# Kernel tuning notes

Hardware: AMD Instinct MI355X
Metric: run time of the kernel (lower is better)

Reference implementation:

```python
import jax, jax.numpy as jnp
import numpy as np


def setup_inputs() -> dict:
    key = jax.random.key(0)
    k1, k2, k3 = jax.random.split(key, 3)
    bs, chart_len, H = 256, 1024, 256
    num_steps, start_index = 512, 512
    chart = jax.random.normal(k1, (bs, chart_len, 2 * H), dtype=jnp.float32)
    operations = jax.random.randint(k2, (num_steps, bs, 2), 0, start_index, dtype=jnp.int64)
    U = jax.random.normal(k3, (5 * H, 2 * H), dtype=jnp.float32) * 0.05
    b = jnp.zeros((5 * H,), dtype=jnp.float32)
    return {"chart": chart, "operations": operations, "start_index": start_index, "U": U, "b": b}


def reference(chart, operations, start_index, U, b):
    H = U.shape[0] // 5
    bs = chart.shape[0]
    batch_idx = jnp.arange(bs)
    num_steps = operations.shape[0]

    def step_fn(ch, xs):
        step, ops = xs
        left = ch[batch_idx, ops[:, 0]]   # [bs, 2H]
        right = ch[batch_idx, ops[:, 1]]  # [bs, 2H]
        ccL, ccR = left[:, :H], right[:, :H]
        hh = jnp.concatenate([left[:, H:], right[:, H:]], axis=-1)  # [bs, 2H]
        preact = hh @ U.T + b  # [bs, 5H]
        i = jax.nn.sigmoid(preact[:, :H])
        fL = jax.nn.sigmoid(preact[:, H:2 * H])
        fR = jax.nn.sigmoid(preact[:, 2 * H:3 * H])
        o = jax.nn.sigmoid(preact[:, 3 * H:4 * H])
        u = jnp.tanh(preact[:, 4 * H:5 * H])
        c = fL * ccL + fR * ccR + i * u
        h = o * jnp.tanh(c)
        ch = ch.at[:, start_index + step, :].set(jnp.concatenate([c, h], axis=-1))
        return ch, None

    chart, _ = jax.lax.scan(step_fn, chart, (jnp.arange(num_steps), operations))
    return chart
```

## Files before the change

### kernel.cpp

```cpp
#include <hip/hip_runtime.h>
#include <hip/hip_bf16.h>

#define H_     256
#define TWOH_  512
#define CL_    1024
#define BS_    256
#define START_ 512

typedef float  f32x16   __attribute__((ext_vector_type(16)));
typedef short  short8_t __attribute__((ext_vector_type(8)));
typedef short  short4_t __attribute__((ext_vector_type(4)));
typedef __bf16 bf16x8   __attribute__((ext_vector_type(8)));

static __device__ __forceinline__ unsigned short f2bf(float x) {
  __hip_bfloat16 h = __float2bfloat16(x);
  return __builtin_bit_cast(unsigned short, h);
}

static __device__ __forceinline__ void gload16(const void* g, void* l) {
  __builtin_amdgcn_global_load_lds(
      (const __attribute__((address_space(1))) void*)g,
      (__attribute__((address_space(3))) void*)l, 16, 0, 0);
}

__global__ void uconv_kernel(const float* __restrict__ U,
                             unsigned short* __restrict__ ub) {
  int tid = blockIdx.x * 256 + threadIdx.x;
  if (tid >= 1280 * 512) return;
  int n = tid >> 9, k = tid & 511;
  int g = n >> 8, j = n & 255;
  int jc = j >> 6, c = (g << 6) + (j & 63);
  ub[((jc * 320 + c) << 9) + k] = f2bf(U[tid]);
}

__global__ void hbconv_kernel(const float* __restrict__ chart,
                              unsigned short* __restrict__ hb) {
  size_t t = (size_t)blockIdx.x * 256 + threadIdx.x;
  size_t row = t >> 5;
  int    kc  = (int)(t & 31) * 8;
  size_t i = row >> 9, pos = row & 511;
  const float* src = chart + (i * CL_ + pos) * TWOH_ + H_ + kc;
  float4 f0 = *(const float4*)(src);
  float4 f1 = *(const float4*)(src + 4);
  short8_t v;
  v[0] = (short)f2bf(f0.x); v[1] = (short)f2bf(f0.y);
  v[2] = (short)f2bf(f0.z); v[3] = (short)f2bf(f0.w);
  v[4] = (short)f2bf(f1.x); v[5] = (short)f2bf(f1.y);
  v[6] = (short)f2bf(f1.z); v[7] = (short)f2bf(f1.w);
  *(short8_t*)(hb + row * H_ + kc) = v;
}

__global__ void copy_kernel(const float4* __restrict__ src,
                            float4* __restrict__ dst) {
  long long tid = (long long)blockIdx.x * blockDim.x + threadIdx.x;
  const long long total = 16777216LL;
  for (long long e = tid; e < total; e += (long long)gridDim.x * blockDim.x) {
    long long i   = e >> 16;
    long long rem = e & 65535;
    long long off = (i << 17) + rem;
    dst[off] = src[off];
  }
}

__global__ __launch_bounds__(256, 2) void chart2_kernel(
    const float* __restrict__ chart,
    const int* __restrict__ ops,
    const unsigned short* __restrict__ ub,
    const unsigned short* __restrict__ hb,
    const float* __restrict__ bias,
    float* __restrict__ out)
{
  __shared__ unsigned short As[2][128 * 32];
  __shared__ unsigned short Bs[2][320 * 32];
  __shared__ int opsl[256];

  const int tid = threadIdx.x, lane = tid & 63, wid = tid >> 6;
  const int l31 = lane & 31, lhi = lane >> 5;
  const int wm = wid & 1, wn = wid >> 1;
  const int bx = blockIdx.x, jc = blockIdx.y;
  const int s = bx >> 1, ibase = (bx & 1) * 128;

  opsl[tid] = ops[(s * BS_ + ibase) * 2 + tid];
  __syncthreads();

  int rA[2], opAL[2], opAR[2], csA[2];
  #pragma unroll
  for (int q = 0; q < 2; ++q) {
    rA[q]   = (wid * 2 + q) * 16 + (lane >> 2);
    opAL[q] = opsl[2 * rA[q]];
    opAR[q] = opsl[2 * rA[q] + 1];
    csA[q]  = (((lane & 3) ^ ((rA[q] >> 1) & 3))) * 8;
  }
  int rB[5], csB[5];
  #pragma unroll
  for (int p = 0; p < 5; ++p) {
    rB[p]  = (wid * 5 + p) * 16 + (lane >> 2);
    csB[p] = (((lane & 3) ^ ((rB[p] >> 1) & 3))) * 8;
  }
  const size_t ub_base = ((size_t)jc * 320) << 9;

  f32x16 acc0[5], acc1[5];
  #pragma unroll
  for (int g = 0; g < 5; ++g)
    #pragma unroll
    for (int q = 0; q < 16; ++q) { acc0[g][q] = 0.f; acc1[g][q] = 0.f; }

#define STAGE(BUF, KT) do {                                                     \
    const int  kt_   = (KT);                                                    \
    const bool left_ = kt_ < 8;                                                 \
    const int  koff_ = left_ ? kt_ * 32 : kt_ * 32 - 256;                       \
    _Pragma("unroll")                                                           \
    for (int q = 0; q < 2; ++q) {                                               \
      int op_ = left_ ? opAL[q] : opAR[q];                                      \
      const unsigned short* g_ =                                                \
          hb + ((size_t)(ibase + rA[q]) * 512 + op_) * 256 + koff_ + csA[q];    \
      gload16(g_, &As[BUF][(wid * 2 + q) * 512]);                               \
    }                                                                           \
    _Pragma("unroll")                                                           \
    for (int p = 0; p < 5; ++p) {                                               \
      const unsigned short* g_ =                                                \
          ub + ub_base + ((size_t)rB[p] << 9) + kt_ * 32 + csB[p];              \
      gload16(g_, &Bs[BUF][(wid * 5 + p) * 512]);                               \
    }                                                                           \
  } while (0)

  STAGE(0, 0);
  __syncthreads();

  const int sw   = (l31 >> 1) & 3;
  const int aro0 = (wm * 64 + l31) * 32;
  const int aro1 = (wm * 64 + 32 + l31) * 32;
  const int bro  = (wn * 32 + l31) * 32;

  int cur = 0;
  for (int kt = 0; kt < 16; ++kt) {
    if (kt + 1 < 16) STAGE(cur ^ 1, kt + 1);
    #pragma unroll
    for (int ks = 0; ks < 2; ++ks) {
      const int ce = ((ks * 2 + lhi) ^ sw) * 8;
      bf16x8 a0 = __builtin_bit_cast(bf16x8, *(const short8_t*)&As[cur][aro0 + ce]);
      bf16x8 a1 = __builtin_bit_cast(bf16x8, *(const short8_t*)&As[cur][aro1 + ce]);
      #pragma unroll
      for (int g = 0; g < 5; ++g) {
        bf16x8 b = __builtin_bit_cast(bf16x8,
            *(const short8_t*)&Bs[cur][bro + g * 2048 + ce]);
        acc0[g] = __builtin_amdgcn_mfma_f32_32x32x16_bf16(a0, b, acc0[g], 0, 0, 0);
        acc1[g] = __builtin_amdgcn_mfma_f32_32x32x16_bf16(a1, b, acc1[g], 0, 0, 0);
      }
    }
    __syncthreads();
    cur ^= 1;
  }
#undef STAGE

  const int jlane = jc * 64 + wn * 32 + l31;
  float bg[5];
  #pragma unroll
  for (int g = 0; g < 5; ++g) bg[g] = bias[g * H_ + jlane];

#define EPI(ACC, M) do {                                                        \
    _Pragma("unroll")                                                           \
    for (int q = 0; q < 16; ++q) {                                              \
      const int row_ = wm * 64 + (M) * 32 + (q & 3) + 8 * (q >> 2) + 4 * lhi;   \
      const int i_   = ibase + row_;                                            \
      const int opL_ = opsl[2 * row_], opR_ = opsl[2 * row_ + 1];               \
      const float ccL_ = chart[((size_t)i_ * CL_ + opL_) * TWOH_ + jlane];      \
      const float ccR_ = chart[((size_t)i_ * CL_ + opR_) * TWOH_ + jlane];      \
      float pi_  = (ACC)[0][q] + bg[0];                                         \
      float pfL_ = (ACC)[1][q] + bg[1];                                         \
      float pfR_ = (ACC)[2][q] + bg[2];                                         \
      float po_  = (ACC)[3][q] + bg[3];                                         \
      float pu_  = (ACC)[4][q] + bg[4];                                         \
      float gi_  = 1.f / (1.f + __expf(-pi_));                                  \
      float gfL_ = 1.f / (1.f + __expf(-pfL_));                                 \
      float gfR_ = 1.f / (1.f + __expf(-pfR_));                                 \
      float go_  = 1.f / (1.f + __expf(-po_));                                  \
      float eu_  = __expf(2.f * pu_);                                           \
      float gu_  = 1.f - 2.f / (eu_ + 1.f);                                     \
      float c_   = gfL_ * ccL_ + gfR_ * ccR_ + gi_ * gu_;                       \
      float ec_  = __expf(2.f * c_);                                            \
      float th_  = 1.f - 2.f / (ec_ + 1.f);                                     \
      float h_   = go_ * th_;                                                   \
      float* orow_ = out + ((size_t)i_ * CL_ + START_ + s) * TWOH_;             \
      orow_[jlane]      = c_;                                                   \
      orow_[H_ + jlane] = h_;                                                   \
    }                                                                           \
  } while (0)

  EPI(acc0, 0);
  EPI(acc1, 1);
#undef EPI
}

__global__ __launch_bounds__(256, 2) void chart1_kernel(
    const float* __restrict__ chart,
    const int* __restrict__ ops,
    const float* __restrict__ U,
    const float* __restrict__ bias,
    float* __restrict__ out)
{
  __shared__ unsigned short As[64 * 72];
  __shared__ unsigned short Bs[320 * 72];
  __shared__ int opsl[128];

  const int tid = threadIdx.x, lane = tid & 63, wid = tid >> 6;
  const int wm = wid & 1, wn = wid >> 1;
  const int bx = blockIdx.x, jc = blockIdx.y;
  const int s = bx >> 2, ibase = (bx & 3) * 64, j0 = jc * 64;

  if (tid < 128) opsl[tid] = ops[(s * BS_ + ibase) * 2 + tid];
  __syncthreads();

  const int arow = tid >> 2, aqc = tid & 3;
  const int opL_s = opsl[2 * arow], opR_s = opsl[2 * arow + 1];
  const long long abase_i = (long long)(ibase + arow) * CL_;

  f32x16 acc[5];
  #pragma unroll
  for (int g = 0; g < 5; ++g)
    #pragma unroll
    for (int q = 0; q < 16; ++q) acc[g][q] = 0.0f;

  const int a_off  = (wm * 32 + (lane & 31)) * 72 + 8 * (lane >> 5);
  const int b_off0 = (wn * 32 + (lane & 31)) * 72 + 8 * (lane >> 5);

  for (int kt = 0; kt < 8; ++kt) {
    const int k0 = kt * 64;
    {
      const int op   = (k0 < 256) ? opL_s : opR_s;
      const int col0 = ((k0 < 256) ? 256 + k0 : k0) + aqc * 16;
      const float* src = chart + (abase_i + op) * TWOH_ + col0;
      float4 f0 = *(const float4*)(src + 0);
      float4 f1 = *(const float4*)(src + 4);
      float4 f2 = *(const float4*)(src + 8);
      float4 f3 = *(const float4*)(src + 12);
      short8_t v0, v1;
      v0[0] = (short)f2bf(f0.x); v0[1] = (short)f2bf(f0.y);
      v0[2] = (short)f2bf(f0.z); v0[3] = (short)f2bf(f0.w);
      v0[4] = (short)f2bf(f1.x); v0[5] = (short)f2bf(f1.y);
      v0[6] = (short)f2bf(f1.z); v0[7] = (short)f2bf(f1.w);
      v1[0] = (short)f2bf(f2.x); v1[1] = (short)f2bf(f2.y);
      v1[2] = (short)f2bf(f2.z); v1[3] = (short)f2bf(f2.w);
      v1[4] = (short)f2bf(f3.x); v1[5] = (short)f2bf(f3.y);
      v1[6] = (short)f2bf(f3.z); v1[7] = (short)f2bf(f3.w);
      *(short8_t*)&As[arow * 72 + aqc * 16]     = v0;
      *(short8_t*)&As[arow * 72 + aqc * 16 + 8] = v1;
    }
    #pragma unroll
    for (int cc = 0; cc < 20; ++cc) {
      int chunk = cc * 256 + tid;
      int c  = chunk >> 4;
      int ko = (chunk & 15) * 4;
      int n  = ((c >> 6) << 8) + j0 + (c & 63);
      float4 f = *(const float4*)(U + (long long)n * 512 + k0 + ko);
      short4_t v;
      v[0] = (short)f2bf(f.x); v[1] = (short)f2bf(f.y);
      v[2] = (short)f2bf(f.z); v[3] = (short)f2bf(f.w);
      *(short4_t*)&Bs[c * 72 + ko] = v;
    }
    __syncthreads();

    #pragma unroll
    for (int ks = 0; ks < 4; ++ks) {
      bf16x8 a = __builtin_bit_cast(bf16x8, *(const short8_t*)&As[a_off + ks * 16]);
      #pragma unroll
      for (int g = 0; g < 5; ++g) {
        bf16x8 b = __builtin_bit_cast(bf16x8,
            *(const short8_t*)&Bs[b_off0 + g * 64 * 72 + ks * 16]);
        acc[g] = __builtin_amdgcn_mfma_f32_32x32x16_bf16(a, b, acc[g], 0, 0, 0);
      }
    }
    __syncthreads();
  }

  const int jlane = j0 + wn * 32 + (lane & 31);
  float bg[5];
  #pragma unroll
  for (int g = 0; g < 5; ++g) bg[g] = bias[g * H_ + jlane];

  #pragma unroll
  for (int q = 0; q < 16; ++q) {
    int rl  = wm * 32 + (q & 3) + 8 * (q >> 2) + 4 * (lane >> 5);
    int i   = ibase + rl;
    int opL = opsl[2 * rl], opR = opsl[2 * rl + 1];
    float ccL = chart[((long long)i * CL_ + opL) * TWOH_ + jlane];
    float ccR = chart[((long long)i * CL_ + opR) * TWOH_ + jlane];
    float pi  = acc[0][q] + bg[0];
    float pfL = acc[1][q] + bg[1];
    float pfR = acc[2][q] + bg[2];
    float po  = acc[3][q] + bg[3];
    float pu  = acc[4][q] + bg[4];
    float gi  = 1.f / (1.f + __expf(-pi));
    float gfL = 1.f / (1.f + __expf(-pfL));
    float gfR = 1.f / (1.f + __expf(-pfR));
    float go  = 1.f / (1.f + __expf(-po));
    float eu  = __expf(2.f * pu);
    float gu  = 1.f - 2.f / (eu + 1.f);
    float c   = gfL * ccL + gfR * ccR + gi * gu;
    float ec  = __expf(2.f * c);
    float th  = 1.f - 2.f / (ec + 1.f);
    float h   = go * th;
    float* orow = out + ((long long)i * CL_ + START_ + s) * TWOH_;
    orow[jlane]      = c;
    orow[H_ + jlane] = h;
  }
}

extern "C" void kernel_launch(void* const* d_in, const int* in_sizes, int n_in,
                              void* d_out, int out_size, void* d_ws, size_t ws_size,
                              hipStream_t stream) {
  const float* chart = (const float*)d_in[0];
  const int*   ops   = (const int*)d_in[1];
  const float* U     = (const float*)d_in[3];
  const float* bias  = (const float*)d_in[4];
  float* out = (float*)d_out;

  copy_kernel<<<4096, 256, 0, stream>>>((const float4*)chart, (float4*)out);

  const size_t UB_BYTES = (size_t)1280 * 512 * 2;
  const size_t HB_OFF   = (size_t)2 << 20;
  const size_t HB_BYTES = (size_t)256 * 512 * 256 * 2;

  if (ws_size >= HB_OFF + HB_BYTES) {
    unsigned short* ub = (unsigned short*)d_ws;
    unsigned short* hb = (unsigned short*)((char*)d_ws + HB_OFF);
    uconv_kernel<<<2560, 256, 0, stream>>>(U, ub);
    hbconv_kernel<<<16384, 256, 0, stream>>>(chart, hb);
    chart2_kernel<<<dim3(1024, 4), 256, 0, stream>>>(chart, ops, ub, hb, bias, out);
  } else {
    chart1_kernel<<<dim3(2048, 4), 256, 0, stream>>>(chart, ops, U, bias, out);
  }
  (void)UB_BYTES;
}
```

Measured before the change: 444.7 us.

## Fuse chart copy into GEMM kernel and deepen K-loop pipeline with explicit waits

Every fifth block of the main kernel now copies the unmodified chart rows to the output, so the standalone copy kernel is gone and its memory traffic overlaps with the MFMA blocks. The K loop now keeps two stages in flight, using explicit vmcnt waits, raw barriers and sched_barrier fences in place of __syncthreads. The ops indices for staging are read straight from global memory, which removes the initial sync. The risks are that copy blocks compete for bandwidth, the grid becomes a 1D decode with a division, and the hand-tuned vmcnt(7) must match the number of loads issued per stage.

```diff
diff --git a/kernel.cpp b/kernel.cpp
--- a/kernel.cpp
+++ b/kernel.cpp
@@ -22,6 +22,8 @@
       (const __attribute__((address_space(1))) void*)g,
       (__attribute__((address_space(3))) void*)l, 16, 0, 0);
 }
+
+#define SCHED0() __builtin_amdgcn_sched_barrier(0)
 
 __global__ void uconv_kernel(const float* __restrict__ U,
                              unsigned short* __restrict__ ub) {
@@ -62,7 +64,7 @@
   }
 }
 
-__global__ __launch_bounds__(256, 2) void chart2_kernel(
+__global__ __launch_bounds__(256, 2) void chart3_kernel(
     const float* __restrict__ chart,
     const int* __restrict__ ops,
     const unsigned short* __restrict__ ub,
@@ -74,21 +76,39 @@
   __shared__ unsigned short Bs[2][320 * 32];
   __shared__ int opsl[256];
 
-  const int tid = threadIdx.x, lane = tid & 63, wid = tid >> 6;
+  const int tid = threadIdx.x;
+  const int bx  = blockIdx.x;
+  const int q5  = bx / 5;
+  const int r5  = bx - q5 * 5;
+
+  if (r5 == 4) {
+    const float4* src = (const float4*)chart;
+    float4* dst = (float4*)out;
+    const long long base = (long long)q5 * 16384 + tid;
+    #pragma unroll 4
+    for (int it = 0; it < 64; ++it) {
+      long long e   = base + it * 256;
+      long long i   = e >> 16;
+      long long rem = e & 65535;
+      long long off = (i << 17) + rem;
+      dst[off] = src[off];
+    }
+    return;
+  }
+
+  const int lane = tid & 63, wid = tid >> 6;
   const int l31 = lane & 31, lhi = lane >> 5;
   const int wm = wid & 1, wn = wid >> 1;
-  const int bx = blockIdx.x, jc = blockIdx.y;
-  const int s = bx >> 1, ibase = (bx & 1) * 128;
+  const int s = q5 >> 1, ibase = (q5 & 1) * 128, jc = r5;
 
   opsl[tid] = ops[(s * BS_ + ibase) * 2 + tid];
-  __syncthreads();
 
   int rA[2], opAL[2], opAR[2], csA[2];
   #pragma unroll
   for (int q = 0; q < 2; ++q) {
     rA[q]   = (wid * 2 + q) * 16 + (lane >> 2);
-    opAL[q] = opsl[2 * rA[q]];
-    opAR[q] = opsl[2 * rA[q] + 1];
+    opAL[q] = ops[(s * BS_ + ibase + rA[q]) * 2];
+    opAR[q] = ops[(s * BS_ + ibase + rA[q]) * 2 + 1];
     csA[q]  = (((lane & 3) ^ ((rA[q] >> 1) & 3))) * 8;
   }
   int rB[5], csB[5];
@@ -124,33 +144,55 @@
     }                                                                           \
   } while (0)
 
-  STAGE(0, 0);
-  __syncthreads();
-
   const int sw   = (l31 >> 1) & 3;
   const int aro0 = (wm * 64 + l31) * 32;
   const int aro1 = (wm * 64 + 32 + l31) * 32;
   const int bro  = (wn * 32 + l31) * 32;
 
-  int cur = 0;
-  for (int kt = 0; kt < 16; ++kt) {
-    if (kt + 1 < 16) STAGE(cur ^ 1, kt + 1);
-    #pragma unroll
-    for (int ks = 0; ks < 2; ++ks) {
-      const int ce = ((ks * 2 + lhi) ^ sw) * 8;
-      bf16x8 a0 = __builtin_bit_cast(bf16x8, *(const short8_t*)&As[cur][aro0 + ce]);
-      bf16x8 a1 = __builtin_bit_cast(bf16x8, *(const short8_t*)&As[cur][aro1 + ce]);
-      #pragma unroll
-      for (int g = 0; g < 5; ++g) {
-        bf16x8 b = __builtin_bit_cast(bf16x8,
-            *(const short8_t*)&Bs[cur][bro + g * 2048 + ce]);
-        acc0[g] = __builtin_amdgcn_mfma_f32_32x32x16_bf16(a0, b, acc0[g], 0, 0, 0);
-        acc1[g] = __builtin_amdgcn_mfma_f32_32x32x16_bf16(a1, b, acc1[g], 0, 0, 0);
-      }
-    }
-    __syncthreads();
-    cur ^= 1;
-  }
+#define COMPUTE(BUF) do {                                                       \
+    _Pragma("unroll")                                                           \
+    for (int ks = 0; ks < 2; ++ks) {                                            \
+      const int ce = ((ks * 2 + lhi) ^ sw) * 8;                                 \
+      bf16x8 a0 = __builtin_bit_cast(bf16x8,                                    \
+          *(const short8_t*)&As[BUF][aro0 + ce]);                               \
+      bf16x8 a1 = __builtin_bit_cast(bf16x8,                                    \
+          *(const short8_t*)&As[BUF][aro1 + ce]);                               \
+      _Pragma("unroll")                                                         \
+      for (int g = 0; g < 5; ++g) {                                             \
+        bf16x8 b = __builtin_bit_cast(bf16x8,                                   \
+            *(const short8_t*)&Bs[BUF][bro + g * 2048 + ce]);                   \
+        acc0[g] = __builtin_amdgcn_mfma_f32_32x32x16_bf16(a0, b, acc0[g],0,0,0);\
+        acc1[g] = __builtin_amdgcn_mfma_f32_32x32x16_bf16(a1, b, acc1[g],0,0,0);\
+      }                                                                         \
+    }                                                                           \
+  } while (0)
+
+#define PHASE(BUF, KT, DOSTAGE) do {                                            \
+    asm volatile("s_waitcnt vmcnt(7)" ::: "memory");                            \
+    __builtin_amdgcn_s_barrier();                                               \
+    SCHED0();                                                                   \
+    COMPUTE(BUF);                                                               \
+    SCHED0();                                                                   \
+    __builtin_amdgcn_s_barrier();                                               \
+    SCHED0();                                                                   \
+    if (DOSTAGE) { STAGE(BUF, (KT) + 2); SCHED0(); }                            \
+  } while (0)
+
+  STAGE(0, 0); SCHED0();
+  STAGE(1, 1); SCHED0();
+
+  for (int kt = 0; kt < 14; kt += 2) {
+    PHASE(0, kt,     true);
+    PHASE(1, kt + 1, true);
+  }
+  PHASE(0, 14, false);
+  asm volatile("s_waitcnt vmcnt(0)" ::: "memory");
+  __builtin_amdgcn_s_barrier();
+  SCHED0();
+  COMPUTE(1);
+
+#undef PHASE
+#undef COMPUTE
 #undef STAGE
 
   const int jlane = jc * 64 + wn * 32 + l31;
@@ -315,9 +357,6 @@
   const float* bias  = (const float*)d_in[4];
   float* out = (float*)d_out;
 
-  copy_kernel<<<4096, 256, 0, stream>>>((const float4*)chart, (float4*)out);
-
-  const size_t UB_BYTES = (size_t)1280 * 512 * 2;
   const size_t HB_OFF   = (size_t)2 << 20;
   const size_t HB_BYTES = (size_t)256 * 512 * 256 * 2;
 
@@ -326,9 +365,9 @@
     unsigned short* hb = (unsigned short*)((char*)d_ws + HB_OFF);
     uconv_kernel<<<2560, 256, 0, stream>>>(U, ub);
     hbconv_kernel<<<16384, 256, 0, stream>>>(chart, hb);
-    chart2_kernel<<<dim3(1024, 4), 256, 0, stream>>>(chart, ops, ub, hb, bias, out);
+    chart3_kernel<<<5120, 256, 0, stream>>>(chart, ops, ub, hb, bias, out);
   } else {
+    copy_kernel<<<4096, 256, 0, stream>>>((const float4*)chart, (float4*)out);
     chart1_kernel<<<dim3(2048, 4), 256, 0, stream>>>(chart, ops, U, bias, out);
   }
-  (void)UB_BYTES;
-}
+}
```

Result: no change. 438.9 us (-1.3%).
